# Kernel tuning notes

Hardware: AMD Instinct MI355X
Metric: run time of the kernel (lower is better)

The kernel has to match this reference:

```python
import jax, jax.numpy as jnp
import numpy as np

# static config (matches init_kwargs)
PL, LAT, LON = 8, 48, 96
WP, WL, WW = 2, 6, 12
SP, SL, SN = 1, 3, 6
NH = 16


def _earth_position_index(ws):
    wp, wl, ww = ws
    zi = np.arange(wp); zj = -np.arange(wp) * wp
    hi = np.arange(wl); hj = -np.arange(wl) * wl
    w = np.arange(ww)
    c1 = np.stack(np.meshgrid(zi, hi, w, indexing='ij')).reshape(3, -1)
    c2 = np.stack(np.meshgrid(zj, hj, w, indexing='ij')).reshape(3, -1)
    coords = (c1[:, :, None] - c2[:, None, :]).transpose(1, 2, 0).astype(np.int64)
    coords[:, :, 2] += ww - 1
    coords[:, :, 1] *= 2 * ww - 1
    coords[:, :, 0] *= (2 * ww - 1) * wl * wl
    return coords.sum(-1)  # (N, N)

_POS_IDX = jnp.asarray(_earth_position_index((WP, WL, WW)))


def _ln(x, w, b, eps=1e-5):
    m = x.mean(-1, keepdims=True)
    v = x.var(-1, keepdims=True)
    return (x - m) / jnp.sqrt(v + eps) * w + b


def setup_inputs() -> dict:
    key = jax.random.key(0)
    ks = jax.random.split(key, 8)
    B, C = 1, 512
    L = PL * LAT * LON
    TOW = (PL // WP) * (LAT // WL)
    TBL = WP * WP * WL * WL * (2 * WW - 1)
    s = 0.02
    return {
        'x': jax.random.normal(ks[0], (B, L, C), jnp.float32),
        'norm1_w': jnp.ones((C,), jnp.float32), 'norm1_b': jnp.zeros((C,), jnp.float32),
        'qkv_w': jax.random.normal(ks[1], (C, 3 * C), jnp.float32) * s,
        'qkv_b': jnp.zeros((3 * C,), jnp.float32),
        'proj_w': jax.random.normal(ks[2], (C, C), jnp.float32) * s,
        'proj_b': jnp.zeros((C,), jnp.float32),
        'bias_table': jax.random.normal(ks[3], (TBL, TOW, NH), jnp.float32) * s,
        'norm2_w': jnp.ones((C,), jnp.float32), 'norm2_b': jnp.zeros((C,), jnp.float32),
        'mlp_w1': jax.random.normal(ks[4], (C, 4 * C), jnp.float32) * s,
        'mlp_b1': jnp.zeros((4 * C,), jnp.float32),
        'mlp_w2': jax.random.normal(ks[5], (4 * C, C), jnp.float32) * s,
        'mlp_b2': jnp.zeros((C,), jnp.float32),
    }


def reference(x, norm1_w, norm1_b, qkv_w, qkv_b, proj_w, proj_b, bias_table,
              norm2_w, norm2_b, mlp_w1, mlp_b1, mlp_w2, mlp_b2):
    B, L, C = x.shape
    HD = C // NH
    scale = HD ** -0.5
    N = WP * WL * WW
    nPl, nLat, nLon = PL // WP, LAT // WL, LON // WW
    nW = nPl * nLat

    # norm1 + roll + window partition (B, nLon, nPl, nLat, wp, wl, ww, C)
    h = _ln(x, norm1_w, norm1_b).reshape(B, PL, LAT, LON, C)
    h = jnp.roll(h, (-SP, -SL, -SN), axis=(1, 2, 3))
    h = h.reshape(B, nPl, WP, nLat, WL, nLon, WW, C)
    h = h.transpose(0, 5, 1, 3, 2, 4, 6, 7).reshape(B * nLon, nW, N, C)

    # attention
    qkv = (h @ qkv_w + qkv_b).reshape(B * nLon, nW, N, 3, NH, HD)
    qkv = qkv.transpose(3, 0, 4, 1, 2, 5)  # (3, B_, nh, nW, N, hd)
    q, k, v = qkv[0] * scale, qkv[1], qkv[2]
    attn = jnp.einsum('bhwnd,bhwmd->bhwnm', q, k)
    bias = bias_table[_POS_IDX.reshape(-1)].reshape(N, N, nW, NH)
    bias = bias.transpose(3, 2, 0, 1)  # (nh, nW, N, N)
    attn = jax.nn.softmax(attn + bias[None], axis=-1)
    o = jnp.einsum('bhwnm,bhwmd->bhwnd', attn, v)
    o = o.transpose(0, 2, 3, 1, 4).reshape(B * nLon, nW, N, C)
    o = o @ proj_w + proj_b

    # reverse partition + roll back
    o = o.reshape(B, nLon, nPl, nLat, WP, WL, WW, C)
    o = o.transpose(0, 2, 4, 3, 5, 1, 6, 7).reshape(B, PL, LAT, LON, C)
    o = jnp.roll(o, (SP, SL, SN), axis=(1, 2, 3)).reshape(B, L, C)

    x = x + o
    h2 = _ln(x, norm2_w, norm2_b)
    h2 = jax.nn.gelu(h2 @ mlp_w1 + mlp_b1, approximate=False) @ mlp_w2 + mlp_b2
    return x + h2
```

## Files before the change

### kernel.cpp

```cpp
#include <hip/hip_runtime.h>
#include <hip/hip_bf16.h>
#include <math.h>

typedef __bf16 bf16;
typedef __attribute__((ext_vector_type(8))) __bf16 bf16x8;
typedef __attribute__((ext_vector_type(4))) float f32x4;
typedef __attribute__((ext_vector_type(8))) float f32x8;

#define NTOK   36864
#define CDIM   512
#define NHEAD  16
#define HD     32
#define NWIN   32
#define NLON   8
#define WTOK   144
#define TBL    3312

#define GLOAD_LDS16(g, l) __builtin_amdgcn_global_load_lds( \
    (const __attribute__((address_space(1))) void*)(const void*)(g), \
    (__attribute__((address_space(3))) void*)(l), 16, 0, 0)

__device__ __forceinline__ int src_token(int r) {
    int ww_ = r % 12; int q = r / 12;
    int wl_ = q % 6;  q /= 6;
    int wp_ = q & 1;  q >>= 1;
    int lat_g = q & 7; q >>= 3;
    int pl_g = q & 3;  q >>= 2;
    int lon_g = q;
    int pl  = pl_g * 2 + wp_ + 1;  if (pl  >= 8)  pl  -= 8;
    int lat = lat_g * 6 + wl_ + 3; if (lat >= 48) lat -= 48;
    int lon = lon_g * 12 + ww_ + 6; if (lon >= 96) lon -= 96;
    return (pl * 48 + lat) * 96 + lon;
}

__device__ __forceinline__ float gelu_exact(float x) {
    return 0.5f * x * (1.0f + erff(x * 0.70710678118654752f));
}

__global__ __launch_bounds__(256) void transpose_f32_bf16(const float* __restrict__ in,
                                                          bf16* __restrict__ out,
                                                          int R, int Cc) {
    __shared__ bf16 tile[32][33];
    int c0 = blockIdx.x * 32, r0 = blockIdx.y * 32;
    int tx = threadIdx.x & 31, ty = threadIdx.x >> 5;
#pragma unroll
    for (int i = 0; i < 32; i += 8)
        tile[ty + i][tx] = (bf16)in[(size_t)(r0 + ty + i) * Cc + c0 + tx];
    __syncthreads();
#pragma unroll
    for (int i = 0; i < 32; i += 8)
        out[(size_t)(c0 + ty + i) * R + r0 + tx] = tile[tx][ty + i];
}

__global__ __launch_bounds__(256) void table_transpose(const float* __restrict__ in,
                                                       float* __restrict__ outT) {
    __shared__ float tile[32][33];
    int i0 = blockIdx.x * 32, w0 = blockIdx.y * 32;
    int tx = threadIdx.x & 31, ty = threadIdx.x >> 5;
#pragma unroll
    for (int r = 0; r < 32; r += 8)
        if (i0 + ty + r < TBL) tile[ty + r][tx] = in[(size_t)(i0 + ty + r) * 512 + w0 + tx];
    __syncthreads();
#pragma unroll
    for (int r = 0; r < 32; r += 8)
        if (i0 + tx < TBL) outT[(size_t)(w0 + ty + r) * TBL + i0 + tx] = tile[tx][ty + r];
}

template<bool PERM>
__global__ __launch_bounds__(256) void ln_kernel(const float* __restrict__ in,
                                                 const float* __restrict__ w,
                                                 const float* __restrict__ b,
                                                 bf16* __restrict__ out) {
    int r = blockIdx.x * 4 + (threadIdx.x >> 6);
    int lane = threadIdx.x & 63;
    int s = PERM ? src_token(r) : r;
    f32x8 v8 = *(const f32x8*)(in + (size_t)s * CDIM + lane * 8);
    float sum = 0.f, sq = 0.f;
#pragma unroll
    for (int i = 0; i < 8; ++i) { sum += v8[i]; sq += v8[i] * v8[i]; }
#pragma unroll
    for (int m = 1; m < 64; m <<= 1) { sum += __shfl_xor(sum, m); sq += __shfl_xor(sq, m); }
    float mean = sum * (1.f / 512.f);
    float var  = sq  * (1.f / 512.f) - mean * mean;
    float rstd = rsqrtf(var + 1e-5f);
    f32x8 w8 = *(const f32x8*)(w + lane * 8);
    f32x8 b8 = *(const f32x8*)(b + lane * 8);
    bf16x8 o8;
#pragma unroll
    for (int i = 0; i < 8; ++i)
        o8[i] = (bf16)((v8[i] - mean) * rstd * w8[i] + b8[i]);
    *(bf16x8*)(out + (size_t)r * CDIM + lane * 8) = o8;
}

template<int EPI>
__global__ __launch_bounds__(256) void gemm_bt(const bf16* __restrict__ A,
                                               const bf16* __restrict__ Bt,
                                               const float* __restrict__ bias,
                                               void* __restrict__ Cout_,
                                               const float* __restrict__ X,
                                               int K, int N) {
    __shared__ bf16 As[128 * 32];
    __shared__ bf16 Bs[128 * 32];
    int t = threadIdx.x;
    int wid = t >> 6, lane = t & 63;
    int wr = wid >> 1, wc = wid & 1;
    int g = lane >> 4, cl = lane & 15;
    int m0 = blockIdx.y * 128, n0 = blockIdx.x * 128;
    f32x4 acc[4][4] = {};

    int srow = wid * 16 + (lane >> 2);
    int scol = (lane & 3) * 8;
    const bf16* Ag0 = A  + (size_t)(m0 + srow) * K + scol;
    const bf16* Ag1 = Ag0 + (size_t)64 * K;
    const bf16* Bg0 = Bt + (size_t)(n0 + srow) * K + scol;
    const bf16* Bg1 = Bg0 + (size_t)64 * K;
    bf16* Al0 = As + wid * 16 * 32;
    bf16* Al1 = Al0 + 64 * 32;
    bf16* Bl0 = Bs + wid * 16 * 32;
    bf16* Bl1 = Bl0 + 64 * 32;

    for (int k0 = 0; k0 < K; k0 += 32) {
        __syncthreads();
        GLOAD_LDS16(Ag0 + k0, Al0);
        GLOAD_LDS16(Ag1 + k0, Al1);
        GLOAD_LDS16(Bg0 + k0, Bl0);
        GLOAD_LDS16(Bg1 + k0, Bl1);
        __syncthreads();
        bf16x8 af[4], bfv[4];
#pragma unroll
        for (int i = 0; i < 4; ++i)
            af[i]  = *(const bf16x8*)(As + (wr * 64 + i * 16 + cl) * 32 + g * 8);
#pragma unroll
        for (int i = 0; i < 4; ++i)
            bfv[i] = *(const bf16x8*)(Bs + (wc * 64 + i * 16 + cl) * 32 + g * 8);
#pragma unroll
        for (int mi = 0; mi < 4; ++mi)
#pragma unroll
            for (int ni = 0; ni < 4; ++ni)
                acc[mi][ni] = __builtin_amdgcn_mfma_f32_16x16x32_bf16(af[mi], bfv[ni], acc[mi][ni], 0, 0, 0);
    }

#pragma unroll
    for (int mi = 0; mi < 4; ++mi) {
#pragma unroll
        for (int j = 0; j < 4; ++j) {
            int row = m0 + wr * 64 + mi * 16 + g * 4 + j;
            int srw = 0;
            if (EPI == 2) srw = src_token(row);
#pragma unroll
            for (int ni = 0; ni < 4; ++ni) {
                int col = n0 + wc * 64 + ni * 16 + cl;
                float v = acc[mi][ni][j] + bias[col];
                if (EPI == 1) v = gelu_exact(v);
                if (EPI == 0 || EPI == 1) {
                    ((bf16*)Cout_)[(size_t)row * N + col] = (bf16)v;
                } else if (EPI == 2) {
                    size_t o = (size_t)srw * CDIM + col;
                    ((float*)Cout_)[o] = X[o] + v;
                } else {
                    size_t o = (size_t)row * N + col;
                    ((float*)Cout_)[o] += v;
                }
            }
        }
    }
}

__global__ __launch_bounds__(256) void attn_mfma(const bf16* __restrict__ qkv,
                                                 const float* __restrict__ tableT,
                                                 bf16* __restrict__ obuf) {
    int h = blockIdx.x, w = blockIdx.y, b_ = blockIdx.z;
    int t = threadIdx.x, wid = t >> 6, lane = t & 63;
    int g = lane >> 4, cl = lane & 15;
    size_t base = ((size_t)b_ * NWIN + w) * WTOK;

    __shared__ bf16 P[WTOK * 168];
    __shared__ bf16 vT[32 * 168];
    __shared__ float bias_s[TBL];
    bf16* qs = P;
    bf16* ks = P + WTOK * 40;

    const bf16* qg = qkv + base * 1536 + h * 32;
    for (int tok = t >> 2; tok < WTOK; tok += 64) {
        int c8 = (t & 3) * 8;
        *(bf16x8*)(qs + tok * 40 + c8) = *(const bf16x8*)(qg + (size_t)tok * 1536 + c8);
        *(bf16x8*)(ks + tok * 40 + c8) = *(const bf16x8*)(qg + 512 + (size_t)tok * 1536 + c8);
        bf16x8 v8 = *(const bf16x8*)(qg + 1024 + (size_t)tok * 1536 + c8);
#pragma unroll
        for (int i = 0; i < 8; ++i) vT[(c8 + i) * 168 + tok] = v8[i];
    }
    for (int z = t; z < 32 * 24; z += 256) vT[(z / 24) * 168 + 144 + (z % 24)] = (bf16)0.f;
    const float* tb = tableT + (size_t)(w * 16 + h) * TBL;
    for (int i = t; i < TBL; i += 256) bias_s[i] = tb[i];
    __syncthreads();

    f32x4 sacc[3][9] = {};
    bf16x8 kf[9];
#pragma unroll
    for (int ct = 0; ct < 9; ++ct)
        kf[ct] = *(const bf16x8*)(ks + (ct * 16 + cl) * 40 + g * 8);
#pragma unroll
    for (int rti = 0; rti < 3; ++rti) {
        int rt = wid + rti * 4;
        if (rt < 9) {
            bf16x8 qf = *(const bf16x8*)(qs + (rt * 16 + cl) * 40 + g * 8);
#pragma unroll
            for (int ct = 0; ct < 9; ++ct)
                sacc[rti][ct] = __builtin_amdgcn_mfma_f32_16x16x32_bf16(qf, kf[ct], sacc[rti][ct], 0, 0, 0);
        }
    }
    __syncthreads();

    for (int z = t; z < WTOK * 24; z += 256) P[(z / 24) * 168 + 144 + (z % 24)] = (bf16)0.f;

    int bm[9];
#pragma unroll
    for (int ct = 0; ct < 9; ++ct) {
        int m = ct * 16 + cl;
        int wm = m % 12, tm = m / 12, hm = tm % 6, zm = tm / 6;
        bm[ct] = zm * 1656 + hm * 138 + 11 - wm;
    }

    const float scale = 0.17677669529663689f;
    float rinv[3][4];
#pragma unroll
    for (int rti = 0; rti < 3; ++rti) {
        int rt = wid + rti * 4;
        if (rt < 9) {
#pragma unroll
            for (int j = 0; j < 4; ++j) {
                int row = rt * 16 + g * 4 + j;
                int wn = row % 12, tn = row / 12, hn = tn % 6, zn = tn / 6;
                int an = zn * 828 + hn * 23 + wn;
                float mx = -1e30f;
#pragma unroll
                for (int ct = 0; ct < 9; ++ct) {
                    float v = sacc[rti][ct][j] * scale + bias_s[an + bm[ct]];
                    sacc[rti][ct][j] = v;
                    mx = fmaxf(mx, v);
                }
                for (int msk = 1; msk < 16; msk <<= 1) mx = fmaxf(mx, __shfl_xor(mx, msk));
                float sm = 0.f;
#pragma unroll
                for (int ct = 0; ct < 9; ++ct) {
                    float p = __expf(sacc[rti][ct][j] - mx);
                    sm += p;
                    P[row * 168 + ct * 16 + cl] = (bf16)p;
                }
                for (int msk = 1; msk < 16; msk <<= 1) sm += __shfl_xor(sm, msk);
                rinv[rti][j] = 1.f / sm;
            }
        }
    }
    __syncthreads();

#pragma unroll
    for (int rti = 0; rti < 3; ++rti) {
        int rt = wid + rti * 4;
        if (rt < 9) {
            f32x4 oacc[2] = {};
#pragma unroll
            for (int ks_ = 0; ks_ < 5; ++ks_) {
                bf16x8 pf = *(const bf16x8*)(P + (rt * 16 + cl) * 168 + ks_ * 32 + g * 8);
#pragma unroll
                for (int c2 = 0; c2 < 2; ++c2) {
                    bf16x8 vf = *(const bf16x8*)(vT + (c2 * 16 + cl) * 168 + ks_ * 32 + g * 8);
                    oacc[c2] = __builtin_amdgcn_mfma_f32_16x16x32_bf16(pf, vf, oacc[c2], 0, 0, 0);
                }
            }
#pragma unroll
            for (int c2 = 0; c2 < 2; ++c2)
#pragma unroll
                for (int j = 0; j < 4; ++j) {
                    int row = rt * 16 + g * 4 + j;
                    obuf[(base + row) * CDIM + h * 32 + c2 * 16 + cl] =
                        (bf16)(oacc[c2][j] * rinv[rti][j]);
                }
        }
    }
}

extern "C" void kernel_launch(void* const* d_in, const int* in_sizes, int n_in,
                              void* d_out, int out_size, void* d_ws, size_t ws_size,
                              hipStream_t stream) {
    const float* x       = (const float*)d_in[0];
    const float* n1w     = (const float*)d_in[1];
    const float* n1b     = (const float*)d_in[2];
    const float* qkv_w   = (const float*)d_in[3];
    const float* qkv_b   = (const float*)d_in[4];
    const float* proj_w  = (const float*)d_in[5];
    const float* proj_b  = (const float*)d_in[6];
    const float* btab    = (const float*)d_in[7];
    const float* n2w     = (const float*)d_in[8];
    const float* n2b     = (const float*)d_in[9];
    const float* mlp_w1  = (const float*)d_in[10];
    const float* mlp_b1  = (const float*)d_in[11];
    const float* mlp_w2  = (const float*)d_in[12];
    const float* mlp_b2  = (const float*)d_in[13];
    float* out = (float*)d_out;

    const size_t OFF_HBUF = 0;
    const size_t OFF_QKV  = 37748736;
    const size_t OFF_TT   = 150994944;
    const size_t OFF_OBUF = 188743680;
    const size_t OFF_WTQ  = 226492416;
    const size_t OFF_WTP  = 228065280;
    const size_t OFF_WT1  = 228589568;
    const size_t OFF_WT2  = 230686720;
    const size_t NEED     = 232783872;

    if (ws_size < NEED) return;

    char* ws = (char*)d_ws;
    bf16*  hbuf   = (bf16*)(ws + OFF_HBUF);
    bf16*  qkvbuf = (bf16*)(ws + OFF_QKV);
    bf16*  midbuf = qkvbuf;
    float* tableT = (float*)(ws + OFF_TT);
    bf16*  obuf   = (bf16*)(ws + OFF_OBUF);
    bf16*  wtq    = (bf16*)(ws + OFF_WTQ);
    bf16*  wtp    = (bf16*)(ws + OFF_WTP);
    bf16*  wt1    = (bf16*)(ws + OFF_WT1);
    bf16*  wt2    = (bf16*)(ws + OFF_WT2);

    transpose_f32_bf16<<<dim3(1536 / 32, 512 / 32), 256, 0, stream>>>(qkv_w, wtq, 512, 1536);
    transpose_f32_bf16<<<dim3(512 / 32, 512 / 32), 256, 0, stream>>>(proj_w, wtp, 512, 512);
    transpose_f32_bf16<<<dim3(2048 / 32, 512 / 32), 256, 0, stream>>>(mlp_w1, wt1, 512, 2048);
    transpose_f32_bf16<<<dim3(512 / 32, 2048 / 32), 256, 0, stream>>>(mlp_w2, wt2, 2048, 512);
    table_transpose<<<dim3((TBL + 31) / 32, 512 / 32), 256, 0, stream>>>(btab, tableT);

    ln_kernel<true><<<NTOK / 4, 256, 0, stream>>>(x, n1w, n1b, hbuf);

    gemm_bt<0><<<dim3(1536 / 128, NTOK / 128), 256, 0, stream>>>(hbuf, wtq, qkv_b, qkvbuf, nullptr, 512, 1536);

    attn_mfma<<<dim3(NHEAD, NWIN, NLON), 256, 0, stream>>>(qkvbuf, tableT, obuf);

    gemm_bt<2><<<dim3(512 / 128, NTOK / 128), 256, 0, stream>>>(obuf, wtp, proj_b, out, x, 512, 512);

    ln_kernel<false><<<NTOK / 4, 256, 0, stream>>>(out, n2w, n2b, hbuf);

    gemm_bt<1><<<dim3(2048 / 128, NTOK / 128), 256, 0, stream>>>(hbuf, wt1, mlp_b1, midbuf, nullptr, 512, 2048);

    gemm_bt<3><<<dim3(512 / 128, NTOK / 128), 256, 0, stream>>>(midbuf, wt2, mlp_b2, out, nullptr, 2048, 512);
}
```

Baseline: 632.2 us.

## Double-buffer GEMM LDS tiles and remap workgroups across XCDs

The bf16 GEMM kernel now keeps two LDS buffers. It issues the global-to-LDS loads for the next K-tile before computing on the current one, which removes one barrier per iteration and overlaps memory with MFMA work. The launch grid becomes 1D, and block IDs are remapped so that consecutive tiles land on the same XCD (8-way interleave), with the aim of better L2 reuse. LDS use per block doubles, which may lower occupancy.

```diff
diff --git a/kernel.cpp b/kernel.cpp
--- a/kernel.cpp
+++ b/kernel.cpp
@@ -98,14 +98,21 @@
                                                const float* __restrict__ bias,
                                                void* __restrict__ Cout_,
                                                const float* __restrict__ X,
-                                               int K, int N) {
-    __shared__ bf16 As[128 * 32];
-    __shared__ bf16 Bs[128 * 32];
+                                               int K, int N, int gx) {
+    __shared__ bf16 As[2 * 128 * 32];
+    __shared__ bf16 Bs[2 * 128 * 32];
     int t = threadIdx.x;
     int wid = t >> 6, lane = t & 63;
     int wr = wid >> 1, wc = wid & 1;
     int g = lane >> 4, cl = lane & 15;
-    int m0 = blockIdx.y * 128, n0 = blockIdx.x * 128;
+
+    int nwg = gridDim.x, orig = blockIdx.x;
+    int wg = orig;
+    if ((nwg & 7) == 0) {
+        int cpx = nwg >> 3;
+        wg = (orig & 7) * cpx + (orig >> 3);
+    }
+    int m0 = (wg / gx) * 128, n0 = (wg % gx) * 128;
     f32x4 acc[4][4] = {};
 
     int srow = wid * 16 + (lane >> 2);
@@ -114,30 +121,41 @@
     const bf16* Ag1 = Ag0 + (size_t)64 * K;
     const bf16* Bg0 = Bt + (size_t)(n0 + srow) * K + scol;
     const bf16* Bg1 = Bg0 + (size_t)64 * K;
-    bf16* Al0 = As + wid * 16 * 32;
-    bf16* Al1 = Al0 + 64 * 32;
-    bf16* Bl0 = Bs + wid * 16 * 32;
-    bf16* Bl1 = Bl0 + 64 * 32;
-
-    for (int k0 = 0; k0 < K; k0 += 32) {
-        __syncthreads();
-        GLOAD_LDS16(Ag0 + k0, Al0);
-        GLOAD_LDS16(Ag1 + k0, Al1);
-        GLOAD_LDS16(Bg0 + k0, Bl0);
-        GLOAD_LDS16(Bg1 + k0, Bl1);
-        __syncthreads();
+    int ldsoff = wid * 16 * 32;
+
+    GLOAD_LDS16(Ag0, As + ldsoff);
+    GLOAD_LDS16(Ag1, As + 64 * 32 + ldsoff);
+    GLOAD_LDS16(Bg0, Bs + ldsoff);
+    GLOAD_LDS16(Bg1, Bs + 64 * 32 + ldsoff);
+    __syncthreads();
+
+    int nt = K >> 5, cur = 0;
+    for (int kt = 0; kt < nt; ++kt) {
+        if (kt + 1 < nt) {
+            int k1 = (kt + 1) << 5;
+            bf16* Ad = As + (cur ^ 1) * 4096;
+            bf16* Bd = Bs + (cur ^ 1) * 4096;
+            GLOAD_LDS16(Ag0 + k1, Ad + ldsoff);
+            GLOAD_LDS16(Ag1 + k1, Ad + 64 * 32 + ldsoff);
+            GLOAD_LDS16(Bg0 + k1, Bd + ldsoff);
+            GLOAD_LDS16(Bg1 + k1, Bd + 64 * 32 + ldsoff);
+        }
+        const bf16* Ar = As + cur * 4096;
+        const bf16* Br = Bs + cur * 4096;
         bf16x8 af[4], bfv[4];
 #pragma unroll
         for (int i = 0; i < 4; ++i)
-            af[i]  = *(const bf16x8*)(As + (wr * 64 + i * 16 + cl) * 32 + g * 8);
+            af[i]  = *(const bf16x8*)(Ar + (wr * 64 + i * 16 + cl) * 32 + g * 8);
 #pragma unroll
         for (int i = 0; i < 4; ++i)
-            bfv[i] = *(const bf16x8*)(Bs + (wc * 64 + i * 16 + cl) * 32 + g * 8);
+            bfv[i] = *(const bf16x8*)(Br + (wc * 64 + i * 16 + cl) * 32 + g * 8);
 #pragma unroll
         for (int mi = 0; mi < 4; ++mi)
 #pragma unroll
             for (int ni = 0; ni < 4; ++ni)
                 acc[mi][ni] = __builtin_amdgcn_mfma_f32_16x16x32_bf16(af[mi], bfv[ni], acc[mi][ni], 0, 0, 0);
+        __syncthreads();
+        cur ^= 1;
     }
 
 #pragma unroll
@@ -330,15 +348,15 @@
 
     ln_kernel<true><<<NTOK / 4, 256, 0, stream>>>(x, n1w, n1b, hbuf);
 
-    gemm_bt<0><<<dim3(1536 / 128, NTOK / 128), 256, 0, stream>>>(hbuf, wtq, qkv_b, qkvbuf, nullptr, 512, 1536);
+    gemm_bt<0><<<12 * 288, 256, 0, stream>>>(hbuf, wtq, qkv_b, qkvbuf, nullptr, 512, 1536, 12);
 
     attn_mfma<<<dim3(NHEAD, NWIN, NLON), 256, 0, stream>>>(qkvbuf, tableT, obuf);
 
-    gemm_bt<2><<<dim3(512 / 128, NTOK / 128), 256, 0, stream>>>(obuf, wtp, proj_b, out, x, 512, 512);
+    gemm_bt<2><<<4 * 288, 256, 0, stream>>>(obuf, wtp, proj_b, out, x, 512, 512, 4);
 
     ln_kernel<false><<<NTOK / 4, 256, 0, stream>>>(out, n2w, n2b, hbuf);
 
-    gemm_bt<1><<<dim3(2048 / 128, NTOK / 128), 256, 0, stream>>>(hbuf, wt1, mlp_b1, midbuf, nullptr, 512, 2048);
-
-    gemm_bt<3><<<dim3(512 / 128, NTOK / 128), 256, 0, stream>>>(midbuf, wt2, mlp_b2, out, nullptr, 2048, 512);
-}
+    gemm_bt<1><<<16 * 288, 256, 0, stream>>>(hbuf, wt1, mlp_b1, midbuf, nullptr, 512, 2048, 16);
+
+    gemm_bt<3><<<4 * 288, 256, 0, stream>>>(midbuf, wt2, mlp_b2, out, nullptr, 2048, 512, 4);
+}
```

New measurement: 575.8 us. -8.9%, faster.

## Replace 128x128 GEMM with double-buffered 256x256 tile GEMM and XCD-aware block mapping

Applied to the files above, without the earlier changes.

Swaps the simple 128x128-tile, single-buffer GEMM for a 512-thread 256x256-tile kernel with a 64-wide K step. It double-buffers LDS across 128KB so global-to-LDS loads of the next K tile overlap the current MFMAs, and uses explicit waitcnt/barrier/setprio scheduling. Block IDs are remapped so consecutive tiles land on the same XCD for L2 reuse. The larger tiles raise arithmetic intensity but cut grid size (288 blocks for the N=512 GEMMs) and use heavy LDS and register space, which may limit occupancy.

```diff
diff --git a/kernel.cpp b/kernel.cpp
--- a/kernel.cpp
+++ b/kernel.cpp
@@ -93,64 +93,150 @@
 }
 
 template<int EPI>
-__global__ __launch_bounds__(256) void gemm_bt(const bf16* __restrict__ A,
-                                               const bf16* __restrict__ Bt,
-                                               const float* __restrict__ bias,
-                                               void* __restrict__ Cout_,
-                                               const float* __restrict__ X,
-                                               int K, int N) {
-    __shared__ bf16 As[128 * 32];
-    __shared__ bf16 Bs[128 * 32];
-    int t = threadIdx.x;
-    int wid = t >> 6, lane = t & 63;
-    int wr = wid >> 1, wc = wid & 1;
-    int g = lane >> 4, cl = lane & 15;
-    int m0 = blockIdx.y * 128, n0 = blockIdx.x * 128;
-    f32x4 acc[4][4] = {};
-
-    int srow = wid * 16 + (lane >> 2);
-    int scol = (lane & 3) * 8;
-    const bf16* Ag0 = A  + (size_t)(m0 + srow) * K + scol;
-    const bf16* Ag1 = Ag0 + (size_t)64 * K;
-    const bf16* Bg0 = Bt + (size_t)(n0 + srow) * K + scol;
-    const bf16* Bg1 = Bg0 + (size_t)64 * K;
-    bf16* Al0 = As + wid * 16 * 32;
-    bf16* Al1 = Al0 + 64 * 32;
-    bf16* Bl0 = Bs + wid * 16 * 32;
-    bf16* Bl1 = Bl0 + 64 * 32;
-
-    for (int k0 = 0; k0 < K; k0 += 32) {
-        __syncthreads();
-        GLOAD_LDS16(Ag0 + k0, Al0);
-        GLOAD_LDS16(Ag1 + k0, Al1);
-        GLOAD_LDS16(Bg0 + k0, Bl0);
-        GLOAD_LDS16(Bg1 + k0, Bl1);
-        __syncthreads();
-        bf16x8 af[4], bfv[4];
-#pragma unroll
-        for (int i = 0; i < 4; ++i)
-            af[i]  = *(const bf16x8*)(As + (wr * 64 + i * 16 + cl) * 32 + g * 8);
-#pragma unroll
-        for (int i = 0; i < 4; ++i)
-            bfv[i] = *(const bf16x8*)(Bs + (wc * 64 + i * 16 + cl) * 32 + g * 8);
-#pragma unroll
-        for (int mi = 0; mi < 4; ++mi)
-#pragma unroll
-            for (int ni = 0; ni < 4; ++ni)
-                acc[mi][ni] = __builtin_amdgcn_mfma_f32_16x16x32_bf16(af[mi], bfv[ni], acc[mi][ni], 0, 0, 0);
-    }
-
-#pragma unroll
-    for (int mi = 0; mi < 4; ++mi) {
-#pragma unroll
-        for (int j = 0; j < 4; ++j) {
-            int row = m0 + wr * 64 + mi * 16 + g * 4 + j;
+__global__ __launch_bounds__(512, 2) void gemm256(const bf16* __restrict__ A,
+                                                  const bf16* __restrict__ Bt,
+                                                  const float* __restrict__ bias,
+                                                  void* __restrict__ Cout_,
+                                                  const float* __restrict__ X,
+                                                  int K, int N, int gx) {
+    __shared__ char lds[131072];
+    const int t = threadIdx.x;
+    const int wid = t >> 6, lane = t & 63;
+    const int wr = wid >> 2, wc = wid & 3;
+    const int g = lane >> 4, cl = lane & 15;
+
+    const int nwg = gridDim.x, orig = blockIdx.x;
+    const int cpx = nwg >> 3;
+    const int wg = (orig & 7) * cpx + (orig >> 3);
+    const int m0 = (wg / gx) * 256, n0 = (wg % gx) * 256;
+
+    f32x4 acc[8][4] = {};
+
+    const size_t rowK128 = (size_t)128 * K;
+    const bf16* Asrc = A  + (size_t)(m0 + wid * 16 + cl) * K + g * 8;
+    const bf16* Bsrc = Bt + (size_t)(n0 + wid * 16 + cl) * K + g * 8;
+    const int ldst = wid << 10;
+    const int lrd  = lane << 4;
+
+    GLOAD_LDS16(Asrc,                lds + 0     + ldst);
+    GLOAD_LDS16(Asrc + rowK128,      lds + 8192  + ldst);
+    GLOAD_LDS16(Bsrc,                lds + 32768 + ldst);
+    GLOAD_LDS16(Bsrc + rowK128,      lds + 40960 + ldst);
+    GLOAD_LDS16(Asrc + 32,           lds + 16384 + ldst);
+    GLOAD_LDS16(Asrc + rowK128 + 32, lds + 24576 + ldst);
+    GLOAD_LDS16(Bsrc + 32,           lds + 49152 + ldst);
+    GLOAD_LDS16(Bsrc + rowK128 + 32, lds + 57344 + ldst);
+    asm volatile("s_waitcnt vmcnt(4)" ::: "memory");
+    __builtin_amdgcn_s_barrier();
+
+    const int NT = K >> 6;
+    for (int tau = 0; tau < NT; ++tau) {
+        const int rd = (tau & 1) << 16;
+        const int st = ((tau + 1) & 1) << 16;
+        const bool stg  = (tau + 1 < NT);
+        const bool last = (tau == NT - 1);
+        const char* Ard = lds + rd;
+        const char* Brd = lds + rd + 32768;
+        char* Ast = lds + st;
+        char* Bst = lds + st + 32768;
+        const bf16* AsS = Asrc + (size_t)(tau + 1) * 64;
+        const bf16* BsS = Bsrc + (size_t)(tau + 1) * 64;
+
+        bf16x8 aF[4], bF[4];
+
+#pragma unroll
+        for (int j = 0; j < 4; ++j)
+            aF[j] = *(const bf16x8*)(Ard + ((wr * 8 + j) << 10) + lrd);
+#pragma unroll
+        for (int fc = 0; fc < 4; ++fc)
+            bF[fc] = *(const bf16x8*)(Brd + ((wc * 4 + fc) << 10) + lrd);
+        if (stg) {
+            GLOAD_LDS16(AsS,           Ast + ldst);
+            GLOAD_LDS16(AsS + rowK128, Ast + 8192 + ldst);
+        }
+        __builtin_amdgcn_s_barrier();
+        asm volatile("s_waitcnt lgkmcnt(0)" ::: "memory");
+        __builtin_amdgcn_s_setprio(1);
+#pragma unroll
+        for (int j = 0; j < 4; ++j)
+#pragma unroll
+            for (int fc = 0; fc < 4; ++fc)
+                acc[j][fc] = __builtin_amdgcn_mfma_f32_16x16x32_bf16(aF[j], bF[fc], acc[j][fc], 0, 0, 0);
+        __builtin_amdgcn_s_setprio(0);
+        __builtin_amdgcn_s_barrier();
+
+#pragma unroll
+        for (int j = 0; j < 4; ++j)
+            aF[j] = *(const bf16x8*)(Ard + ((wr * 8 + 4 + j) << 10) + lrd);
+        if (stg) {
+            GLOAD_LDS16(BsS,           Bst + ldst);
+            GLOAD_LDS16(BsS + rowK128, Bst + 8192 + ldst);
+        }
+        if (last) asm volatile("s_waitcnt vmcnt(0)" ::: "memory");
+        else      asm volatile("s_waitcnt vmcnt(4)" ::: "memory");
+        __builtin_amdgcn_s_barrier();
+        asm volatile("s_waitcnt lgkmcnt(0)" ::: "memory");
+        __builtin_amdgcn_s_setprio(1);
+#pragma unroll
+        for (int j = 0; j < 4; ++j)
+#pragma unroll
+            for (int fc = 0; fc < 4; ++fc)
+                acc[4 + j][fc] = __builtin_amdgcn_mfma_f32_16x16x32_bf16(aF[j], bF[fc], acc[4 + j][fc], 0, 0, 0);
+        __builtin_amdgcn_s_setprio(0);
+        __builtin_amdgcn_s_barrier();
+
+#pragma unroll
+        for (int j = 0; j < 4; ++j)
+            aF[j] = *(const bf16x8*)(Ard + 16384 + ((wr * 8 + j) << 10) + lrd);
+#pragma unroll
+        for (int fc = 0; fc < 4; ++fc)
+            bF[fc] = *(const bf16x8*)(Brd + 16384 + ((wc * 4 + fc) << 10) + lrd);
+        if (stg) {
+            GLOAD_LDS16(AsS + 32,           Ast + 16384 + ldst);
+            GLOAD_LDS16(AsS + rowK128 + 32, Ast + 24576 + ldst);
+        }
+        __builtin_amdgcn_s_barrier();
+        asm volatile("s_waitcnt lgkmcnt(0)" ::: "memory");
+        __builtin_amdgcn_s_setprio(1);
+#pragma unroll
+        for (int j = 0; j < 4; ++j)
+#pragma unroll
+            for (int fc = 0; fc < 4; ++fc)
+                acc[j][fc] = __builtin_amdgcn_mfma_f32_16x16x32_bf16(aF[j], bF[fc], acc[j][fc], 0, 0, 0);
+        __builtin_amdgcn_s_setprio(0);
+        __builtin_amdgcn_s_barrier();
+
+#pragma unroll
+        for (int j = 0; j < 4; ++j)
+            aF[j] = *(const bf16x8*)(Ard + 16384 + ((wr * 8 + 4 + j) << 10) + lrd);
+        if (stg) {
+            GLOAD_LDS16(BsS + 32,           Bst + 16384 + ldst);
+            GLOAD_LDS16(BsS + rowK128 + 32, Bst + 24576 + ldst);
+        }
+        if (!last) asm volatile("s_waitcnt vmcnt(4)" ::: "memory");
+        __builtin_amdgcn_s_barrier();
+        asm volatile("s_waitcnt lgkmcnt(0)" ::: "memory");
+        __builtin_amdgcn_s_setprio(1);
+#pragma unroll
+        for (int j = 0; j < 4; ++j)
+#pragma unroll
+            for (int fc = 0; fc < 4; ++fc)
+                acc[4 + j][fc] = __builtin_amdgcn_mfma_f32_16x16x32_bf16(aF[j], bF[fc], acc[4 + j][fc], 0, 0, 0);
+        __builtin_amdgcn_s_setprio(0);
+        __builtin_amdgcn_s_barrier();
+    }
+
+#pragma unroll
+    for (int fr = 0; fr < 8; ++fr) {
+#pragma unroll
+        for (int jj = 0; jj < 4; ++jj) {
+            int row = m0 + wr * 128 + fr * 16 + g * 4 + jj;
             int srw = 0;
             if (EPI == 2) srw = src_token(row);
 #pragma unroll
-            for (int ni = 0; ni < 4; ++ni) {
-                int col = n0 + wc * 64 + ni * 16 + cl;
-                float v = acc[mi][ni][j] + bias[col];
+            for (int fc = 0; fc < 4; ++fc) {
+                int col = n0 + wc * 64 + fc * 16 + cl;
+                float v = acc[fr][fc][jj] + bias[col];
                 if (EPI == 1) v = gelu_exact(v);
                 if (EPI == 0 || EPI == 1) {
                     ((bf16*)Cout_)[(size_t)row * N + col] = (bf16)v;
@@ -330,15 +416,15 @@
 
     ln_kernel<true><<<NTOK / 4, 256, 0, stream>>>(x, n1w, n1b, hbuf);
 
-    gemm_bt<0><<<dim3(1536 / 128, NTOK / 128), 256, 0, stream>>>(hbuf, wtq, qkv_b, qkvbuf, nullptr, 512, 1536);
+    gemm256<0><<<864, 512, 0, stream>>>(hbuf, wtq, qkv_b, qkvbuf, nullptr, 512, 1536, 6);
 
     attn_mfma<<<dim3(NHEAD, NWIN, NLON), 256, 0, stream>>>(qkvbuf, tableT, obuf);
 
-    gemm_bt<2><<<dim3(512 / 128, NTOK / 128), 256, 0, stream>>>(obuf, wtp, proj_b, out, x, 512, 512);
+    gemm256<2><<<288, 512, 0, stream>>>(obuf, wtp, proj_b, out, x, 512, 512, 2);
 
     ln_kernel<false><<<NTOK / 4, 256, 0, stream>>>(out, n2w, n2b, hbuf);
 
-    gemm_bt<1><<<dim3(2048 / 128, NTOK / 128), 256, 0, stream>>>(hbuf, wt1, mlp_b1, midbuf, nullptr, 512, 2048);
-
-    gemm_bt<3><<<dim3(512 / 128, NTOK / 128), 256, 0, stream>>>(midbuf, wt2, mlp_b2, out, nullptr, 2048, 512);
-}
+    gemm256<1><<<1152, 512, 0, stream>>>(hbuf, wt1, mlp_b1, midbuf, nullptr, 512, 2048, 8);
+
+    gemm256<3><<<288, 512, 0, stream>>>(midbuf, wt2, mlp_b2, out, nullptr, 2048, 512, 2);
+}
```

Measured after the change: 659.9 us. +4.4%, slower.
